# Performance work log

Hardware: AMD Instinct MI355X
Metric: run time of the kernel (lower is better)

## Reference

```python
import jax, jax.numpy as jnp
import numpy as np

NUM_ROUTING = 3


def squash(x):
    # norm along last dim, scale = n/(1+n), direction x/sqrt(n+1e-8)
    norm = jnp.sum(x * x, axis=-1, keepdims=True)
    scale = norm / (1.0 + norm)
    return scale * (x / jnp.sqrt(norm + 1e-8))


def setup_inputs() -> dict:
    key = jax.random.key(0)
    k1, k2 = jax.random.split(key)
    B, C, h, w = 32, 8, 24, 24          # B must equal num_routes=32; h*w must equal num_classes
    num_classes = 576                    # == h*w (required by torch.matmul broadcasting)
    x = jax.random.normal(k1, (B, C, h, w), dtype=jnp.float32)
    route_weights = jax.random.normal(k2, (32, num_classes, 8, 16), dtype=jnp.float32)
    return {"x": x, "route_weights": route_weights}


def reference(x, route_weights):
    B, C, h, w = x.shape                 # C == 8
    R = h * w                            # routes (spatial), == num_caps
    K = route_weights.shape[1]           # num_capsules (== R)
    D = route_weights.shape[3]           # 16

    # [B, C, h, w] -> [B, R, 8]
    x2 = jnp.transpose(x.reshape(B, C, R), (0, 2, 1))

    # torch broadcasting aligns (B, R) with W's (32, num_caps):
    # u_hat[b, r, i, j] = sum_k x2[b, r, k] * W[b, r, k, j]   (constant over i)
    u_core = jnp.einsum('brk,brkj->brj', x2, route_weights)   # [B, R, D]
    u_hat = jnp.broadcast_to(u_core[:, :, None, :], (B, R, K, D))

    b = jnp.zeros((B, R, K), dtype=x.dtype)
    v = None
    for i in range(NUM_ROUTING):
        c = jax.nn.softmax(b, axis=2)                         # over capsule axis
        s = jnp.einsum('bri,brij->bij', c, u_hat)             # sum over routes r -> [B, K, D]
        v = squash(s)
        if i < NUM_ROUTING - 1:
            b = b + jnp.einsum('brij,bij->bri', u_hat, v)     # agreement update
    return v
```

## Files before the change

### kernel.cpp

```cpp
#include <hip/hip_runtime.h>


#define NB 32
#define NR 576
#define NC 8
#define ND 16
#define NBLK 9

__global__ __launch_bounds__(64) void caps_partial(const float* __restrict__ x,
                                                   const float* __restrict__ W,
                                                   float* __restrict__ partial) {
    const int b    = blockIdx.x;
    const int blk  = blockIdx.y;
    const int lane = threadIdx.x;
    const int r    = blk * 64 + lane;

    const float* xb = x + (size_t)b * NC * NR;
    const float* Wr = W + ((size_t)b * NR + r) * NC * ND;

    float xv[NC];
#pragma unroll
    for (int k = 0; k < NC; ++k) xv[k] = xb[k * NR + r];

    float acc[ND];
#pragma unroll
    for (int j = 0; j < ND; ++j) acc[j] = 0.f;

#pragma unroll
    for (int k = 0; k < NC; ++k) {
        const float4 w0 = *reinterpret_cast<const float4*>(Wr + k * ND + 0);
        const float4 w1 = *reinterpret_cast<const float4*>(Wr + k * ND + 4);
        const float4 w2 = *reinterpret_cast<const float4*>(Wr + k * ND + 8);
        const float4 w3 = *reinterpret_cast<const float4*>(Wr + k * ND + 12);
        const float xk = xv[k];
        acc[0]  += xk * w0.x;  acc[1]  += xk * w0.y;
        acc[2]  += xk * w0.z;  acc[3]  += xk * w0.w;
        acc[4]  += xk * w1.x;  acc[5]  += xk * w1.y;
        acc[6]  += xk * w1.z;  acc[7]  += xk * w1.w;
        acc[8]  += xk * w2.x;  acc[9]  += xk * w2.y;
        acc[10] += xk * w2.z;  acc[11] += xk * w2.w;
        acc[12] += xk * w3.x;  acc[13] += xk * w3.y;
        acc[14] += xk * w3.z;  acc[15] += xk * w3.w;
    }

#pragma unroll
    for (int j = 0; j < ND; ++j) {
        for (int m = 1; m < 64; m <<= 1)
            acc[j] += __shfl_xor(acc[j], m, 64);
    }

    if (lane == 0) {
        float* p = partial + ((size_t)b * NBLK + blk) * ND;
#pragma unroll
        for (int j = 0; j < ND; ++j) p[j] = acc[j];
    }
}

__global__ __launch_bounds__(256) void caps_finish(const float* __restrict__ partial,
                                                   float* __restrict__ out) {
    const int b   = blockIdx.x;
    const int tid = threadIdx.x;

    float s[ND];
#pragma unroll
    for (int j = 0; j < ND; ++j) s[j] = 0.f;
    const float* p = partial + (size_t)b * NBLK * ND;
    for (int q = 0; q < NBLK; ++q) {
#pragma unroll
        for (int j = 0; j < ND; ++j) s[j] += p[q * ND + j];
    }

    const float cmean = 1.0f / 576.0f;
    float norm = 0.f;
#pragma unroll
    for (int j = 0; j < ND; ++j) { s[j] *= cmean; norm += s[j] * s[j]; }

    const float sc = norm / ((1.0f + norm) * sqrtf(norm + 1e-8f));

    float v[ND];
#pragma unroll
    for (int j = 0; j < ND; ++j) v[j] = s[j] * sc;

    const float4 q0 = make_float4(v[0],  v[1],  v[2],  v[3]);
    const float4 q1 = make_float4(v[4],  v[5],  v[6],  v[7]);
    const float4 q2 = make_float4(v[8],  v[9],  v[10], v[11]);
    const float4 q3 = make_float4(v[12], v[13], v[14], v[15]);

    const int qi = tid & 3;
    const float4 vq = (qi == 0) ? q0 : (qi == 1) ? q1 : (qi == 2) ? q2 : q3;

    float4* ob = reinterpret_cast<float4*>(out + (size_t)b * NR * ND);
#pragma unroll
    for (int sdx = 0; sdx < 9; ++sdx) ob[tid + 256 * sdx] = vq;
}

extern "C" void kernel_launch(void* const* d_in, const int* in_sizes, int n_in,
                              void* d_out, int out_size, void* d_ws, size_t ws_size,
                              hipStream_t stream) {
    const float* x = (const float*)d_in[0];
    const float* W = (const float*)d_in[1];
    float* out     = (float*)d_out;
    float* partial = (float*)d_ws;

    dim3 gridA(NB, NBLK);
    caps_partial<<<gridA, 64, 0, stream>>>(x, W, partial);
    caps_finish<<<NB, 256, 0, stream>>>(partial, out);
}
```

Baseline: 11.74 us.

## Fuse partial reduction and squash/broadcast into one 576-thread block per batch

Merges the two kernels into one launch: each batch gets a 576-thread block whose 9 wavefronts reduce into shared memory, then all threads compute squash and write the broadcast output. This removes the second launch and the global partial-buffer round trip. In exchange, only 32 blocks run, versus 288 small blocks before, so fewer CUs pull the weight data in parallel. The output write loop is re-indexed for 576 threads.

After: 16.44 us. 1.4x slower.

```diff
diff --git a/kernel.cpp b/kernel.cpp
--- a/kernel.cpp
+++ b/kernel.cpp
@@ -5,15 +5,18 @@
 #define NR 576
 #define NC 8
 #define ND 16
-#define NBLK 9
+#define NW 9
 
-__global__ __launch_bounds__(64) void caps_partial(const float* __restrict__ x,
-                                                   const float* __restrict__ W,
-                                                   float* __restrict__ partial) {
+__global__ __launch_bounds__(NR) void caps_fused(const float* __restrict__ x,
+                                                 const float* __restrict__ W,
+                                                 float* __restrict__ out) {
     const int b    = blockIdx.x;
-    const int blk  = blockIdx.y;
-    const int lane = threadIdx.x;
-    const int r    = blk * 64 + lane;
+    const int tid  = threadIdx.x;
+    const int wid  = tid >> 6;
+    const int lane = tid & 63;
+    const int r    = tid;
+
+    __shared__ float part[NW * ND];
 
     const float* xb = x + (size_t)b * NC * NR;
     const float* Wr = W + ((size_t)b * NR + r) * NC * ND;
@@ -45,29 +48,24 @@
 
 #pragma unroll
     for (int j = 0; j < ND; ++j) {
+#pragma unroll
         for (int m = 1; m < 64; m <<= 1)
             acc[j] += __shfl_xor(acc[j], m, 64);
     }
 
     if (lane == 0) {
-        float* p = partial + ((size_t)b * NBLK + blk) * ND;
 #pragma unroll
-        for (int j = 0; j < ND; ++j) p[j] = acc[j];
+        for (int j = 0; j < ND; ++j) part[wid * ND + j] = acc[j];
     }
-}
-
-__global__ __launch_bounds__(256) void caps_finish(const float* __restrict__ partial,
-                                                   float* __restrict__ out) {
-    const int b   = blockIdx.x;
-    const int tid = threadIdx.x;
+    __syncthreads();
 
     float s[ND];
 #pragma unroll
     for (int j = 0; j < ND; ++j) s[j] = 0.f;
-    const float* p = partial + (size_t)b * NBLK * ND;
-    for (int q = 0; q < NBLK; ++q) {
 #pragma unroll
-        for (int j = 0; j < ND; ++j) s[j] += p[q * ND + j];
+    for (int q = 0; q < NW; ++q) {
+#pragma unroll
+        for (int j = 0; j < ND; ++j) s[j] += part[q * ND + j];
     }
 
     const float cmean = 1.0f / 576.0f;
@@ -91,7 +89,7 @@
 
     float4* ob = reinterpret_cast<float4*>(out + (size_t)b * NR * ND);
 #pragma unroll
-    for (int sdx = 0; sdx < 9; ++sdx) ob[tid + 256 * sdx] = vq;
+    for (int sdx = 0; sdx < 4; ++sdx) ob[tid + NR * sdx] = vq;
 }
 
 extern "C" void kernel_launch(void* const* d_in, const int* in_sizes, int n_in,
@@ -100,9 +98,6 @@
     const float* x = (const float*)d_in[0];
     const float* W = (const float*)d_in[1];
     float* out     = (float*)d_out;
-    float* partial = (float*)d_ws;
 
-    dim3 gridA(NB, NBLK);
-    caps_partial<<<gridA, 64, 0, stream>>>(x, W, partial);
-    caps_finish<<<NB, 256, 0, stream>>>(partial, out);
+    caps_fused<<<NB, NR, 0, stream>>>(x, W, out);
 }
```
